# Kernel tuning notes

Hardware: AMD Instinct MI355X
Metric: run time of the kernel (lower is better)

The kernel has to match this reference:

```python
import jax, jax.numpy as jnp
import numpy as np

N_NODES, N_EDGES, NFEAT, NHID, PROHID, NCLASS = 50000, 800000, 500, 128, 512, 10


def _gcn_layer(x, W, b, src, dst, dinv):
    # PyG GCNConv: x' = D^-1/2 (A+I) D^-1/2 (x W) + b, messages src -> dst
    xw = x @ W  # [N, out]
    norm = dinv[src] * dinv[dst]  # [E+N]
    msg = xw[src] * norm[:, None]  # [E+N, out]
    return jax.ops.segment_sum(msg, dst, num_segments=x.shape[0]) + b


def setup_inputs() -> dict:
    key = jax.random.key(0)
    ks = jax.random.split(key, 16)

    def lin(k, fan_in, fan_out):
        bound = 1.0 / np.sqrt(fan_in)
        kw, kb = jax.random.split(k)
        W = jax.random.uniform(kw, (fan_in, fan_out), jnp.float32, -bound, bound)
        b = jax.random.uniform(kb, (fan_out,), jnp.float32, -bound, bound)
        return W, b

    x = jax.random.normal(ks[0], (N_NODES, NFEAT), dtype=jnp.float32)
    edge_index = jax.random.randint(ks[1], (2, N_EDGES), 0, N_NODES, dtype=jnp.int64)

    W1, b1 = lin(ks[2], NFEAT, 2 * NHID)
    W2, b2 = lin(ks[3], 2 * NHID, NHID)
    Wi1, bi1 = lin(ks[4], NHID, PROHID)
    Wi2, bi2 = lin(ks[5], PROHID, NHID)
    Wc1, bc1 = lin(ks[6], NHID, PROHID)
    Wc2, bc2 = lin(ks[7], PROHID, NCLASS)

    return {"x": x, "edge_index": edge_index,
            "W1": W1, "b1": b1, "W2": W2, "b2": b2,
            "Wi1": Wi1, "bi1": bi1, "Wi2": Wi2, "bi2": bi2,
            "Wc1": Wc1, "bc1": bc1, "Wc2": Wc2, "bc2": bc2}


def reference(x, edge_index, W1, b1, W2, b2, Wi1, bi1, Wi2, bi2, Wc1, bc1, Wc2, bc2):
    n = x.shape[0]
    loop = jnp.arange(n, dtype=edge_index.dtype)
    src = jnp.concatenate([edge_index[0], loop])  # add self-loops
    dst = jnp.concatenate([edge_index[1], loop])
    deg = jax.ops.segment_sum(jnp.ones_like(src, dtype=x.dtype), dst, num_segments=n)
    dinv = jnp.where(deg > 0, jax.lax.rsqrt(deg), 0.0)

    h = jax.nn.relu(_gcn_layer(x, W1, b1, src, dst, dinv))
    h = jax.nn.relu(_gcn_layer(h, W2, b2, src, dst, dinv))

    zi = jax.nn.relu(h @ Wi1 + bi1) @ Wi2 + bi2
    z = zi / jnp.maximum(jnp.linalg.norm(zi, axis=1, keepdims=True), 1e-12)

    c = jax.nn.softmax(jax.nn.relu(h @ Wc1 + bc1) @ Wc2 + bc2, axis=1)
    return z, c
```

## Files before the change

kernel.cpp:

```cpp
#include <hip/hip_runtime.h>
#include <math.h>

#define NN 50000
#define NE 800000

typedef __attribute__((ext_vector_type(4))) float f32x4;
typedef __attribute__((ext_vector_type(8))) short s16x8;
typedef __attribute__((ext_vector_type(4))) short s16x4;

__device__ inline float wave_sum(float v) {
#pragma unroll
  for (int off = 32; off >= 1; off >>= 1) v += __shfl_xor(v, off, 64);
  return v;
}

__device__ inline int xcd_swizzle(int orig, int nwg) {
  int q = nwg >> 3, r = nwg & 7;
  int xcd = orig & 7, pos = orig >> 3;
  return (xcd < r ? xcd * (q + 1) : r * (q + 1) + (xcd - r) * q) + pos;
}

__device__ inline short f2bf(float f) {
  unsigned u = __float_as_uint(f);
  unsigned r = (u + 0x7fffu + ((u >> 16) & 1u)) >> 16;
  return (short)r;
}
__device__ inline float bf2f(short h) {
  return __uint_as_float(((unsigned)(unsigned short)h) << 16);
}

__global__ __launch_bounds__(256) void init_kernel(int* __restrict__ deg,
                                                   int* __restrict__ cursor, int n) {
  int i = blockIdx.x * 256 + threadIdx.x;
  if (i < n) { deg[i] = 1; cursor[i] = 0; }
}

__global__ __launch_bounds__(256) void deg_kernel(const int* __restrict__ ei,
                                                  int* __restrict__ deg) {
  int e = blockIdx.x * 256 + threadIdx.x;
  if (e < NE) atomicAdd(&deg[ei[NE + e]], 1);
}

__global__ __launch_bounds__(256) void dinv_kernel(const int* __restrict__ deg,
                                                   float* __restrict__ dinv, int n) {
  int i = blockIdx.x * 256 + threadIdx.x;
  if (i < n) dinv[i] = rsqrtf((float)deg[i]);
}

__global__ __launch_bounds__(256) void scan_kernel(const int* __restrict__ cnt,
                                                   int* __restrict__ offs, int n) {
  __shared__ int buf0[256], buf1[256];
  int tid = threadIdx.x;
  int per = (n + 255) >> 8;
  int start = tid * per;
  int end = min(start + per, n);
  int s = 0;
  for (int i = start; i < end; ++i) s += cnt[i];
  buf0[tid] = s;
  __syncthreads();
  int* src = buf0;
  int* dst = buf1;
#pragma unroll
  for (int off = 1; off < 256; off <<= 1) {
    int v = src[tid];
    if (tid >= off) v += src[tid - off];
    dst[tid] = v;
    __syncthreads();
    int* t = src; src = dst; dst = t;
  }
  int run = (tid == 0) ? 0 : src[tid - 1];
  for (int i = start; i < end; ++i) { offs[i] = run; run += cnt[i]; }
  if (end == n) offs[n] = run;
}

__global__ __launch_bounds__(256) void scatter_kernel(const int* __restrict__ ei,
                                                      const int* __restrict__ offs,
                                                      int* __restrict__ cursor,
                                                      int* __restrict__ csr) {
  int e = blockIdx.x * 256 + threadIdx.x;
  if (e >= NE + NN) return;
  int s, d;
  if (e < NE) { s = ei[e]; d = ei[NE + e]; }
  else        { s = e - NE; d = s; }
  int pos = atomicAdd(&cursor[d], 1);
  csr[offs[d] + pos] = s;
}

template <int EPI>
__global__ __launch_bounds__(256, 2) void mfma_gemm(const float* __restrict__ A,
                                                    const float* __restrict__ B,
                                                    const float* __restrict__ bias,
                                                    float* __restrict__ C,
                                                    int M, int N, int K, int gn) {
  __shared__ short Ahi[128 * 64], Alo[128 * 64];
  __shared__ short Bhi[128 * 64], Blo[128 * 64];
  int tid = threadIdx.x;

  int wgid = xcd_swizzle(blockIdx.x, gridDim.x);
  int rb = wgid / gn;
  int cb = wgid - rb * gn;
  int m0 = rb * 128;
  int n0 = cb * 128;

  int wv = tid >> 6, lane = tid & 63;
  int wm = wv >> 1, wn = wv & 1;
  int lrow = lane & 15, lblk = lane >> 4;

  int asr = tid >> 4;
  int ask = tid & 15;
  int bcol = tid & 127;
  int bkh = tid >> 7;

  f32x4 acc[4][4] = {};

  int nt = (K + 63) >> 6;
  for (int t0 = 0; t0 < nt; ++t0) {
    int k0 = t0 << 6;
    __syncthreads();
#pragma unroll
    for (int p = 0; p < 8; ++p) {
      int row = p * 16 + asr;
      int gm = m0 + row;
      int gk = k0 + ask * 4;
      float4 v = make_float4(0.f, 0.f, 0.f, 0.f);
      if (gm < M && gk < K) v = *(const float4*)&A[(size_t)gm * K + gk];
      float fv[4] = {v.x, v.y, v.z, v.w};
      s16x4 h, l;
#pragma unroll
      for (int j = 0; j < 4; ++j) {
        short hh = f2bf(fv[j]);
        h[j] = hh;
        l[j] = f2bf(fv[j] - bf2f(hh));
      }
      int idx = row * 64 + ((ask * 4) ^ ((row & 7) << 3));
      *(s16x4*)&Ahi[idx] = h;
      *(s16x4*)&Alo[idx] = l;
    }
#pragma unroll
    for (int j = 0; j < 8; ++j) {
      s16x4 h, l;
#pragma unroll
      for (int i = 0; i < 4; ++i) {
        int kk = bkh * 32 + j * 4 + i;
        int gk = k0 + kk;
        float v = (gk < K) ? B[(size_t)gk * N + n0 + bcol] : 0.f;
        short hh = f2bf(v);
        h[i] = hh;
        l[i] = f2bf(v - bf2f(hh));
      }
      int kkb = bkh * 32 + j * 4;
      int idx = bcol * 64 + (kkb ^ ((bcol & 7) << 3));
      *(s16x4*)&Bhi[idx] = h;
      *(s16x4*)&Blo[idx] = l;
    }
    __syncthreads();
#pragma unroll
    for (int s = 0; s < 2; ++s) {
      s16x8 ah[4], al[4], bh[4], bl[4];
      int kk = s * 32 + lblk * 8;
#pragma unroll
      for (int f = 0; f < 4; ++f) {
        int ra = wm * 64 + f * 16 + lrow;
        int ia = ra * 64 + (kk ^ ((ra & 7) << 3));
        ah[f] = *(const s16x8*)&Ahi[ia];
        al[f] = *(const s16x8*)&Alo[ia];
        int rbn = wn * 64 + f * 16 + lrow;
        int ib = rbn * 64 + (kk ^ ((rbn & 7) << 3));
        bh[f] = *(const s16x8*)&Bhi[ib];
        bl[f] = *(const s16x8*)&Blo[ib];
      }
#pragma unroll
      for (int i = 0; i < 4; ++i)
#pragma unroll
        for (int j = 0; j < 4; ++j) {
          acc[i][j] = __builtin_amdgcn_mfma_f32_16x16x32_bf16(ah[i], bh[j], acc[i][j], 0, 0, 0);
          acc[i][j] = __builtin_amdgcn_mfma_f32_16x16x32_bf16(ah[i], bl[j], acc[i][j], 0, 0, 0);
          acc[i][j] = __builtin_amdgcn_mfma_f32_16x16x32_bf16(al[i], bh[j], acc[i][j], 0, 0, 0);
        }
    }
  }

#pragma unroll
  for (int i = 0; i < 4; ++i) {
    int crow0 = m0 + wm * 64 + i * 16 + lblk * 4;
#pragma unroll
    for (int j = 0; j < 4; ++j) {
      int ccol = n0 + wn * 64 + j * 16 + lrow;
      float bb = EPI ? bias[ccol] : 0.f;
#pragma unroll
      for (int r = 0; r < 4; ++r) {
        int crow = crow0 + r;
        if (crow < M) {
          float v = acc[i][j][r] + bb;
          if (EPI == 1) v = fmaxf(v, 0.f);
          C[(size_t)crow * N + ccol] = v;
        }
      }
    }
  }
}

template <int C>
__global__ __launch_bounds__(256) void agg_kernel(const float* __restrict__ xw,
                                                  const int* __restrict__ offs,
                                                  const int* __restrict__ csr,
                                                  const float* __restrict__ dinv,
                                                  const float* __restrict__ bias,
                                                  float* __restrict__ out) {
  constexpr int TPN = C / 4;
  constexpr int NPB = 256 / TPN;
  int lane = threadIdx.x % TPN;
  int sub  = threadIdx.x / TPN;
  int node = blockIdx.x * NPB + sub;
  if (node >= NN) return;

  const float4* xw4 = (const float4*)xw;
  int beg = offs[node], end = offs[node + 1];
  float4 acc = make_float4(0.f, 0.f, 0.f, 0.f);
  int j = beg;
  for (; j + 2 <= end; j += 2) {
    int s0 = csr[j], s1 = csr[j + 1];
    float d0 = dinv[s0], d1 = dinv[s1];
    float4 v0 = xw4[(size_t)s0 * TPN + lane];
    float4 v1 = xw4[(size_t)s1 * TPN + lane];
    acc.x += d0 * v0.x + d1 * v1.x;
    acc.y += d0 * v0.y + d1 * v1.y;
    acc.z += d0 * v0.z + d1 * v1.z;
    acc.w += d0 * v0.w + d1 * v1.w;
  }
  if (j < end) {
    int s = csr[j];
    float d = dinv[s];
    float4 v = xw4[(size_t)s * TPN + lane];
    acc.x += d * v.x; acc.y += d * v.y; acc.z += d * v.z; acc.w += d * v.w;
  }
  float dn = dinv[node];
  float4 b = ((const float4*)bias)[lane];
  float4 o;
  o.x = fmaxf(dn * acc.x + b.x, 0.f);
  o.y = fmaxf(dn * acc.y + b.y, 0.f);
  o.z = fmaxf(dn * acc.z + b.z, 0.f);
  o.w = fmaxf(dn * acc.w + b.w, 0.f);
  ((float4*)out)[(size_t)node * TPN + lane] = o;
}

__global__ __launch_bounds__(128) void rownorm_kernel(const float* __restrict__ zi,
                                                      float* __restrict__ z) {
  int row = blockIdx.x;
  int t = threadIdx.x;
  float v = zi[(size_t)row * 128 + t];
  float ss = wave_sum(v * v);
  __shared__ float wsum[2];
  if ((t & 63) == 0) wsum[t >> 6] = ss;
  __syncthreads();
  float tot = wsum[0] + wsum[1];
  float rinv = 1.f / fmaxf(sqrtf(tot), 1e-12f);
  z[(size_t)row * 128 + t] = v * rinv;
}

__global__ __launch_bounds__(256) void cls_kernel(const float* __restrict__ c1,
                                                  const float* __restrict__ W,
                                                  const float* __restrict__ bias,
                                                  float* __restrict__ out, int M) {
  __shared__ float Wt[10 * 512];
  int tid = threadIdx.x;
  for (int i = tid; i < 5120; i += 256) Wt[i] = W[(i & 511) * 10 + (i >> 9)];
  __syncthreads();
  int wave = tid >> 6, lane = tid & 63;
  int row0 = blockIdx.x * 16 + wave * 4;
#pragma unroll 1
  for (int r = 0; r < 4; ++r) {
    int row = row0 + r;
    if (row >= M) continue;
    float acc[10] = {};
    const float* xr = c1 + (size_t)row * 512;
    for (int k = lane; k < 512; k += 64) {
      float xv = xr[k];
#pragma unroll
      for (int c = 0; c < 10; ++c) acc[c] += xv * Wt[c * 512 + k];
    }
#pragma unroll
    for (int c = 0; c < 10; ++c) acc[c] = wave_sum(acc[c]);
    float mx = -1e30f;
#pragma unroll
    for (int c = 0; c < 10; ++c) { acc[c] += bias[c]; mx = fmaxf(mx, acc[c]); }
    float sum = 0.f;
#pragma unroll
    for (int c = 0; c < 10; ++c) { acc[c] = expf(acc[c] - mx); sum += acc[c]; }
    float rs = 1.f / sum;
    if (lane < 10) out[(size_t)row * 10 + lane] = acc[lane] * rs;
  }
}

extern "C" void kernel_launch(void* const* d_in, const int* in_sizes, int n_in,
                              void* d_out, int out_size, void* d_ws, size_t ws_size,
                              hipStream_t stream) {
  const float* x   = (const float*)d_in[0];
  const int*   ei  = (const int*)d_in[1];
  const float* W1  = (const float*)d_in[2];
  const float* b1  = (const float*)d_in[3];
  const float* W2  = (const float*)d_in[4];
  const float* b2  = (const float*)d_in[5];
  const float* Wi1 = (const float*)d_in[6];
  const float* bi1 = (const float*)d_in[7];
  const float* Wi2 = (const float*)d_in[8];
  const float* bi2 = (const float*)d_in[9];
  const float* Wc1 = (const float*)d_in[10];
  const float* bc1 = (const float*)d_in[11];
  const float* Wc2 = (const float*)d_in[12];
  const float* bc2 = (const float*)d_in[13];

  float* out_z = (float*)d_out;
  float* out_c = (float*)d_out + (size_t)NN * 128;

  char* ws = (char*)d_ws;
  size_t off = 0;
  auto alloc = [&](size_t bytes) {
    size_t r = off;
    off = (off + bytes + 255) & ~(size_t)255;
    return r;
  };
  int*   deg    = (int*)(ws + alloc((size_t)NN * 4));
  int*   cursor = (int*)(ws + alloc((size_t)NN * 4));
  int*   offs   = (int*)(ws + alloc((size_t)(NN + 1) * 4));
  float* dinv   = (float*)(ws + alloc((size_t)NN * 4));
  int*   csr    = (int*)(ws + alloc((size_t)(NE + NN) * 4));
  float* bufA   = (float*)(ws + alloc((size_t)NN * 256 * 4));
  float* bufB   = (float*)(ws + alloc((size_t)NN * 256 * 4));
  float* bufD   = (float*)(ws + alloc((size_t)NN * 512 * 4));
  (void)ws_size; (void)in_sizes; (void)n_in; (void)out_size;

  const int M = NN;
  const int gmb = (M + 127) / 128;

  init_kernel<<<(NN + 255) / 256, 256, 0, stream>>>(deg, cursor, NN);
  deg_kernel<<<(NE + 255) / 256, 256, 0, stream>>>(ei, deg);
  dinv_kernel<<<(NN + 255) / 256, 256, 0, stream>>>(deg, dinv, NN);
  scan_kernel<<<1, 256, 0, stream>>>(deg, offs, NN);
  scatter_kernel<<<(NE + NN + 255) / 256, 256, 0, stream>>>(ei, offs, cursor, csr);

  dim3 blk(256);
  mfma_gemm<0><<<gmb * 2, blk, 0, stream>>>(x, W1, nullptr, bufA, M, 256, 500, 2);
  agg_kernel<256><<<(NN + 3) / 4, 256, 0, stream>>>(bufA, offs, csr, dinv, b1, bufB);
  mfma_gemm<0><<<gmb * 1, blk, 0, stream>>>(bufB, W2, nullptr, bufA, M, 128, 256, 1);
  agg_kernel<128><<<(NN + 7) / 8, 256, 0, stream>>>(bufA, offs, csr, dinv, b2, bufB);
  mfma_gemm<1><<<gmb * 4, blk, 0, stream>>>(bufB, Wi1, bi1, bufD, M, 512, 128, 4);
  mfma_gemm<2><<<gmb * 1, blk, 0, stream>>>(bufD, Wi2, bi2, bufA, M, 128, 512, 1);
  rownorm_kernel<<<M, 128, 0, stream>>>(bufA, out_z);
  mfma_gemm<1><<<gmb * 4, blk, 0, stream>>>(bufB, Wc1, bc1, bufD, M, 512, 128, 4);
  cls_kernel<<<(M + 15) / 16, 256, 0, stream>>>(bufD, Wc2, bc2, out_c, M);
}
```

Measured before the change: 1.013 ms.

## Pre-split operands into bf16 hi/lo buffers and stream them into GEMM

Moves the fp32-to-bf16 hi/lo split out of the GEMM inner loop. Inputs and weights are converted once by separate kernels, weights are stored transposed and padded to K-major layout, and the aggregation and GEMM epilogues now write hi/lo bf16 pairs directly. The GEMM then only copies pre-split tiles into padded LDS (K-step 32, stride 40 instead of an XOR swizzle) and raises occupancy to 4 blocks per CU. The aim is to remove repeated conversion work and uncoalesced weight loads from the GEMMs. The cost is extra conversion launches and an extra pass over x, plus more K-loop iterations with smaller tiles.

```diff
diff --git a/kernel.cpp b/kernel.cpp
--- a/kernel.cpp
+++ b/kernel.cpp
@@ -86,14 +86,61 @@
   csr[offs[d] + pos] = s;
 }
 
-template <int EPI>
-__global__ __launch_bounds__(256, 2) void mfma_gemm(const float* __restrict__ A,
-                                                    const float* __restrict__ B,
-                                                    const float* __restrict__ bias,
-                                                    float* __restrict__ C,
-                                                    int M, int N, int K, int gn) {
-  __shared__ short Ahi[128 * 64], Alo[128 * 64];
-  __shared__ short Bhi[128 * 64], Blo[128 * 64];
+__global__ __launch_bounds__(256) void convert_a(const float* __restrict__ in,
+                                                 short* __restrict__ hi,
+                                                 short* __restrict__ lo,
+                                                 int M, int K, int KP) {
+  int t = blockIdx.x * 256 + threadIdx.x;
+  int perRow = KP >> 3;
+  int row = t / perRow;
+  if (row >= M) return;
+  int k8 = (t - row * perRow) << 3;
+  s16x8 h, l;
+#pragma unroll
+  for (int j = 0; j < 8; ++j) {
+    int k = k8 + j;
+    float v = (k < K) ? in[(size_t)row * K + k] : 0.f;
+    short hh = f2bf(v);
+    h[j] = hh;
+    l[j] = f2bf(v - bf2f(hh));
+  }
+  *(s16x8*)&hi[(size_t)row * KP + k8] = h;
+  *(s16x8*)&lo[(size_t)row * KP + k8] = l;
+}
+
+__global__ __launch_bounds__(256) void convert_w(const float* __restrict__ B,
+                                                 short* __restrict__ hi,
+                                                 short* __restrict__ lo,
+                                                 int K, int N, int KP) {
+  int t = blockIdx.x * 256 + threadIdx.x;
+  int perRow = KP >> 3;
+  int col = t / perRow;
+  if (col >= N) return;
+  int k8 = (t - col * perRow) << 3;
+  s16x8 h, l;
+#pragma unroll
+  for (int j = 0; j < 8; ++j) {
+    int k = k8 + j;
+    float v = (k < K) ? B[(size_t)k * N + col] : 0.f;
+    short hh = f2bf(v);
+    h[j] = hh;
+    l[j] = f2bf(v - bf2f(hh));
+  }
+  *(s16x8*)&hi[(size_t)col * KP + k8] = h;
+  *(s16x8*)&lo[(size_t)col * KP + k8] = l;
+}
+
+#define LDSW 40
+
+template <int EPI, int OUTF32>
+__global__ __launch_bounds__(256, 4) void mfma_gemm(
+    const short* __restrict__ Ah, const short* __restrict__ Al,
+    const short* __restrict__ Bh, const short* __restrict__ Bl,
+    const float* __restrict__ bias,
+    float* __restrict__ C, short* __restrict__ Ch, short* __restrict__ Cl,
+    int M, int N, int KP, int gn) {
+  __shared__ short sAh[128 * LDSW], sAl[128 * LDSW];
+  __shared__ short sBh[128 * LDSW], sBl[128 * LDSW];
   int tid = threadIdx.x;
 
   int wgid = xcd_swizzle(blockIdx.x, gridDim.x);
@@ -102,81 +149,49 @@
   int m0 = rb * 128;
   int n0 = cb * 128;
 
-  int wv = tid >> 6, lane = tid & 63;
+  int lane = tid & 63, wv = tid >> 6;
   int wm = wv >> 1, wn = wv & 1;
   int lrow = lane & 15, lblk = lane >> 4;
 
-  int asr = tid >> 4;
-  int ask = tid & 15;
-  int bcol = tid & 127;
-  int bkh = tid >> 7;
+  int srow = tid >> 2;
+  int sslot = tid & 3;
 
   f32x4 acc[4][4] = {};
 
-  int nt = (K + 63) >> 6;
-  for (int t0 = 0; t0 < nt; ++t0) {
-    int k0 = t0 << 6;
+  for (int k0 = 0; k0 < KP; k0 += 32) {
     __syncthreads();
 #pragma unroll
-    for (int p = 0; p < 8; ++p) {
-      int row = p * 16 + asr;
-      int gm = m0 + row;
-      int gk = k0 + ask * 4;
-      float4 v = make_float4(0.f, 0.f, 0.f, 0.f);
-      if (gm < M && gk < K) v = *(const float4*)&A[(size_t)gm * K + gk];
-      float fv[4] = {v.x, v.y, v.z, v.w};
-      s16x4 h, l;
-#pragma unroll
-      for (int j = 0; j < 4; ++j) {
-        short hh = f2bf(fv[j]);
-        h[j] = hh;
-        l[j] = f2bf(fv[j] - bf2f(hh));
-      }
-      int idx = row * 64 + ((ask * 4) ^ ((row & 7) << 3));
-      *(s16x4*)&Ahi[idx] = h;
-      *(s16x4*)&Alo[idx] = l;
-    }
-#pragma unroll
-    for (int j = 0; j < 8; ++j) {
-      s16x4 h, l;
-#pragma unroll
-      for (int i = 0; i < 4; ++i) {
-        int kk = bkh * 32 + j * 4 + i;
-        int gk = k0 + kk;
-        float v = (gk < K) ? B[(size_t)gk * N + n0 + bcol] : 0.f;
-        short hh = f2bf(v);
-        h[i] = hh;
-        l[i] = f2bf(v - bf2f(hh));
-      }
-      int kkb = bkh * 32 + j * 4;
-      int idx = bcol * 64 + (kkb ^ ((bcol & 7) << 3));
-      *(s16x4*)&Bhi[idx] = h;
-      *(s16x4*)&Blo[idx] = l;
+    for (int i = 0; i < 2; ++i) {
+      int row = srow + i * 64;
+      int lds = row * LDSW + sslot * 8;
+      size_t ga = (size_t)(m0 + row) * KP + k0 + sslot * 8;
+      s16x8 vh = {}, vl = {};
+      if (m0 + row < M) { vh = *(const s16x8*)&Ah[ga]; vl = *(const s16x8*)&Al[ga]; }
+      *(s16x8*)&sAh[lds] = vh;
+      *(s16x8*)&sAl[lds] = vl;
+      size_t gb = (size_t)(n0 + row) * KP + k0 + sslot * 8;
+      *(s16x8*)&sBh[lds] = *(const s16x8*)&Bh[gb];
+      *(s16x8*)&sBl[lds] = *(const s16x8*)&Bl[gb];
     }
     __syncthreads();
-#pragma unroll
-    for (int s = 0; s < 2; ++s) {
-      s16x8 ah[4], al[4], bh[4], bl[4];
-      int kk = s * 32 + lblk * 8;
-#pragma unroll
-      for (int f = 0; f < 4; ++f) {
-        int ra = wm * 64 + f * 16 + lrow;
-        int ia = ra * 64 + (kk ^ ((ra & 7) << 3));
-        ah[f] = *(const s16x8*)&Ahi[ia];
-        al[f] = *(const s16x8*)&Alo[ia];
-        int rbn = wn * 64 + f * 16 + lrow;
-        int ib = rbn * 64 + (kk ^ ((rbn & 7) << 3));
-        bh[f] = *(const s16x8*)&Bhi[ib];
-        bl[f] = *(const s16x8*)&Blo[ib];
+    s16x8 ah[4], al[4];
+#pragma unroll
+    for (int f = 0; f < 4; ++f) {
+      int o = (wm * 64 + f * 16 + lrow) * LDSW + lblk * 8;
+      ah[f] = *(const s16x8*)&sAh[o];
+      al[f] = *(const s16x8*)&sAl[o];
+    }
+#pragma unroll
+    for (int j = 0; j < 4; ++j) {
+      int o = (wn * 64 + j * 16 + lrow) * LDSW + lblk * 8;
+      s16x8 bh = *(const s16x8*)&sBh[o];
+      s16x8 bl = *(const s16x8*)&sBl[o];
+#pragma unroll
+      for (int i = 0; i < 4; ++i) {
+        acc[i][j] = __builtin_amdgcn_mfma_f32_16x16x32_bf16(ah[i], bh, acc[i][j], 0, 0, 0);
+        acc[i][j] = __builtin_amdgcn_mfma_f32_16x16x32_bf16(ah[i], bl, acc[i][j], 0, 0, 0);
+        acc[i][j] = __builtin_amdgcn_mfma_f32_16x16x32_bf16(al[i], bh, acc[i][j], 0, 0, 0);
       }
-#pragma unroll
-      for (int i = 0; i < 4; ++i)
-#pragma unroll
-        for (int j = 0; j < 4; ++j) {
-          acc[i][j] = __builtin_amdgcn_mfma_f32_16x16x32_bf16(ah[i], bh[j], acc[i][j], 0, 0, 0);
-          acc[i][j] = __builtin_amdgcn_mfma_f32_16x16x32_bf16(ah[i], bl[j], acc[i][j], 0, 0, 0);
-          acc[i][j] = __builtin_amdgcn_mfma_f32_16x16x32_bf16(al[i], bh[j], acc[i][j], 0, 0, 0);
-        }
     }
   }
 
@@ -190,10 +205,15 @@
 #pragma unroll
       for (int r = 0; r < 4; ++r) {
         int crow = crow0 + r;
-        if (crow < M) {
-          float v = acc[i][j][r] + bb;
-          if (EPI == 1) v = fmaxf(v, 0.f);
+        if (crow >= M) continue;
+        float v = acc[i][j][r] + bb;
+        if (EPI == 1) v = fmaxf(v, 0.f);
+        if (OUTF32) {
           C[(size_t)crow * N + ccol] = v;
+        } else {
+          short hh = f2bf(v);
+          Ch[(size_t)crow * N + ccol] = hh;
+          Cl[(size_t)crow * N + ccol] = f2bf(v - bf2f(hh));
         }
       }
     }
@@ -206,7 +226,8 @@
                                                   const int* __restrict__ csr,
                                                   const float* __restrict__ dinv,
                                                   const float* __restrict__ bias,
-                                                  float* __restrict__ out) {
+                                                  short* __restrict__ oh,
+                                                  short* __restrict__ ol) {
   constexpr int TPN = C / 4;
   constexpr int NPB = 256 / TPN;
   int lane = threadIdx.x % TPN;
@@ -236,12 +257,20 @@
   }
   float dn = dinv[node];
   float4 b = ((const float4*)bias)[lane];
-  float4 o;
-  o.x = fmaxf(dn * acc.x + b.x, 0.f);
-  o.y = fmaxf(dn * acc.y + b.y, 0.f);
-  o.z = fmaxf(dn * acc.z + b.z, 0.f);
-  o.w = fmaxf(dn * acc.w + b.w, 0.f);
-  ((float4*)out)[(size_t)node * TPN + lane] = o;
+  float o[4];
+  o[0] = fmaxf(dn * acc.x + b.x, 0.f);
+  o[1] = fmaxf(dn * acc.y + b.y, 0.f);
+  o[2] = fmaxf(dn * acc.z + b.z, 0.f);
+  o[3] = fmaxf(dn * acc.w + b.w, 0.f);
+  s16x4 h, l;
+#pragma unroll
+  for (int q = 0; q < 4; ++q) {
+    short hh = f2bf(o[q]);
+    h[q] = hh;
+    l[q] = f2bf(o[q] - bf2f(hh));
+  }
+  *(s16x4*)&oh[(size_t)node * C + lane * 4] = h;
+  *(s16x4*)&ol[(size_t)node * C + lane * 4] = l;
 }
 
 __global__ __launch_bounds__(128) void rownorm_kernel(const float* __restrict__ zi,
@@ -258,7 +287,8 @@
   z[(size_t)row * 128 + t] = v * rinv;
 }
 
-__global__ __launch_bounds__(256) void cls_kernel(const float* __restrict__ c1,
+__global__ __launch_bounds__(256) void cls_kernel(const short* __restrict__ c1h,
+                                                  const short* __restrict__ c1l,
                                                   const float* __restrict__ W,
                                                   const float* __restrict__ bias,
                                                   float* __restrict__ out, int M) {
@@ -268,16 +298,19 @@
   __syncthreads();
   int wave = tid >> 6, lane = tid & 63;
   int row0 = blockIdx.x * 16 + wave * 4;
+  int k8 = lane * 8;
 #pragma unroll 1
   for (int r = 0; r < 4; ++r) {
     int row = row0 + r;
     if (row >= M) continue;
     float acc[10] = {};
-    const float* xr = c1 + (size_t)row * 512;
-    for (int k = lane; k < 512; k += 64) {
-      float xv = xr[k];
-#pragma unroll
-      for (int c = 0; c < 10; ++c) acc[c] += xv * Wt[c * 512 + k];
+    s16x8 xh = *(const s16x8*)&c1h[(size_t)row * 512 + k8];
+    s16x8 xl = *(const s16x8*)&c1l[(size_t)row * 512 + k8];
+#pragma unroll
+    for (int j = 0; j < 8; ++j) {
+      float xv = bf2f(xh[j]) + bf2f(xl[j]);
+#pragma unroll
+      for (int c = 0; c < 10; ++c) acc[c] += xv * Wt[c * 512 + k8 + j];
     }
 #pragma unroll
     for (int c = 0; c < 10; ++c) acc[c] = wave_sum(acc[c]);
@@ -325,13 +358,28 @@
   int*   offs   = (int*)(ws + alloc((size_t)(NN + 1) * 4));
   float* dinv   = (float*)(ws + alloc((size_t)NN * 4));
   int*   csr    = (int*)(ws + alloc((size_t)(NE + NN) * 4));
-  float* bufA   = (float*)(ws + alloc((size_t)NN * 256 * 4));
-  float* bufB   = (float*)(ws + alloc((size_t)NN * 256 * 4));
-  float* bufD   = (float*)(ws + alloc((size_t)NN * 512 * 4));
+  short* W1th  = (short*)(ws + alloc((size_t)256 * 512 * 2));
+  short* W1tl  = (short*)(ws + alloc((size_t)256 * 512 * 2));
+  short* W2th  = (short*)(ws + alloc((size_t)128 * 256 * 2));
+  short* W2tl  = (short*)(ws + alloc((size_t)128 * 256 * 2));
+  short* Wi1th = (short*)(ws + alloc((size_t)512 * 128 * 2));
+  short* Wi1tl = (short*)(ws + alloc((size_t)512 * 128 * 2));
+  short* Wi2th = (short*)(ws + alloc((size_t)128 * 512 * 2));
+  short* Wi2tl = (short*)(ws + alloc((size_t)128 * 512 * 2));
+  short* Wc1th = (short*)(ws + alloc((size_t)512 * 128 * 2));
+  short* Wc1tl = (short*)(ws + alloc((size_t)512 * 128 * 2));
+  float* bufA = (float*)(ws + alloc((size_t)NN * 256 * 4));
+  short* h1h  = (short*)(ws + alloc((size_t)NN * 256 * 2));
+  short* h1l  = (short*)(ws + alloc((size_t)NN * 256 * 2));
+  short* Dh   = (short*)(ws + alloc((size_t)NN * 512 * 2));
+  short* Dl   = (short*)(ws + alloc((size_t)NN * 512 * 2));
+  short* h2h  = h1h;
+  short* h2l  = h1l;
   (void)ws_size; (void)in_sizes; (void)n_in; (void)out_size;
 
   const int M = NN;
   const int gmb = (M + 127) / 128;
+  dim3 blk(256);
 
   init_kernel<<<(NN + 255) / 256, 256, 0, stream>>>(deg, cursor, NN);
   deg_kernel<<<(NE + 255) / 256, 256, 0, stream>>>(ei, deg);
@@ -339,14 +387,25 @@
   scan_kernel<<<1, 256, 0, stream>>>(deg, offs, NN);
   scatter_kernel<<<(NE + NN + 255) / 256, 256, 0, stream>>>(ei, offs, cursor, csr);
 
-  dim3 blk(256);
-  mfma_gemm<0><<<gmb * 2, blk, 0, stream>>>(x, W1, nullptr, bufA, M, 256, 500, 2);
-  agg_kernel<256><<<(NN + 3) / 4, 256, 0, stream>>>(bufA, offs, csr, dinv, b1, bufB);
-  mfma_gemm<0><<<gmb * 1, blk, 0, stream>>>(bufB, W2, nullptr, bufA, M, 128, 256, 1);
-  agg_kernel<128><<<(NN + 7) / 8, 256, 0, stream>>>(bufA, offs, csr, dinv, b2, bufB);
-  mfma_gemm<1><<<gmb * 4, blk, 0, stream>>>(bufB, Wi1, bi1, bufD, M, 512, 128, 4);
-  mfma_gemm<2><<<gmb * 1, blk, 0, stream>>>(bufD, Wi2, bi2, bufA, M, 128, 512, 1);
+  convert_a<<<(M * (512 / 8) + 255) / 256, 256, 0, stream>>>(x, Dh, Dl, M, 500, 512);
+  convert_w<<<(256 * (512 / 8) + 255) / 256, 256, 0, stream>>>(W1, W1th, W1tl, 500, 256, 512);
+  convert_w<<<(128 * (256 / 8) + 255) / 256, 256, 0, stream>>>(W2, W2th, W2tl, 256, 128, 256);
+  convert_w<<<(512 * (128 / 8) + 255) / 256, 256, 0, stream>>>(Wi1, Wi1th, Wi1tl, 128, 512, 128);
+  convert_w<<<(128 * (512 / 8) + 255) / 256, 256, 0, stream>>>(Wi2, Wi2th, Wi2tl, 512, 128, 512);
+  convert_w<<<(512 * (128 / 8) + 255) / 256, 256, 0, stream>>>(Wc1, Wc1th, Wc1tl, 128, 512, 128);
+
+  mfma_gemm<0, 1><<<gmb * 2, blk, 0, stream>>>(Dh, Dl, W1th, W1tl, nullptr,
+                                               bufA, nullptr, nullptr, M, 256, 512, 2);
+  agg_kernel<256><<<(NN + 3) / 4, 256, 0, stream>>>(bufA, offs, csr, dinv, b1, h1h, h1l);
+  mfma_gemm<0, 1><<<gmb * 1, blk, 0, stream>>>(h1h, h1l, W2th, W2tl, nullptr,
+                                               bufA, nullptr, nullptr, M, 128, 256, 1);
+  agg_kernel<128><<<(NN + 7) / 8, 256, 0, stream>>>(bufA, offs, csr, dinv, b2, h2h, h2l);
+  mfma_gemm<1, 0><<<gmb * 4, blk, 0, stream>>>(h2h, h2l, Wi1th, Wi1tl, bi1,
+                                               nullptr, Dh, Dl, M, 512, 128, 4);
+  mfma_gemm<2, 1><<<gmb * 1, blk, 0, stream>>>(Dh, Dl, Wi2th, Wi2tl, bi2,
+                                               bufA, nullptr, nullptr, M, 128, 512, 1);
   rownorm_kernel<<<M, 128, 0, stream>>>(bufA, out_z);
-  mfma_gemm<1><<<gmb * 4, blk, 0, stream>>>(bufB, Wc1, bc1, bufD, M, 512, 128, 4);
-  cls_kernel<<<(M + 15) / 16, 256, 0, stream>>>(bufD, Wc2, bc2, out_c, M);
-}
+  mfma_gemm<1, 0><<<gmb * 4, blk, 0, stream>>>(h2h, h2l, Wc1th, Wc1tl, bc1,
+                                               nullptr, Dh, Dl, M, 512, 128, 4);
+  cls_kernel<<<(M + 15) / 16, 256, 0, stream>>>(Dh, Dl, Wc2, bc2, out_c, M);
+}
```

Result: faster. 831.5 us (-18.0%).
